# Kernel tuning notes

Measured on AMD Instinct MI355X. Metric: run time of the kernel, lower is better.

Reference implementation:

```python
import jax, jax.numpy as jnp
import numpy as np
from math import sqrt


def setup_inputs() -> dict:
    key = jax.random.key(0)
    kq, kk, kv = jax.random.split(key, 3)
    B, L, H, E = 4, 2048, 8, 64
    S, D = L, E
    return {
        "queries": jax.random.normal(kq, (B, L, H, E), dtype=jnp.float32),
        "keys": jax.random.normal(kk, (B, S, H, E), dtype=jnp.float32),
        "values": jax.random.normal(kv, (B, S, H, D), dtype=jnp.float32),
    }


def reference(queries, keys, values):
    # FullAttention with mask_flag=True (TriangularCausalMask), dropout p=0,
    # output_attention=False. scale = 1/sqrt(E).
    B, L, H, E = queries.shape
    S = keys.shape[1]
    scale = 1.0 / sqrt(E)
    # scores: [B, H, L, S]
    scores = jnp.einsum("blhe,bshe->bhls", queries, keys)
    # causal mask: positions s > l are masked (upper triangle above diagonal)
    causal = jnp.tril(jnp.ones((L, S), dtype=bool))  # True = keep
    neg_inf = jnp.finfo(scores.dtype).min
    scores = jnp.where(causal, scores, neg_inf)
    A = jax.nn.softmax(scale * scores, axis=-1)  # [B,H,L,S]
    # context: [B, L, H, D]
    V = jnp.einsum("bhls,bshd->blhd", A, values)
    return V
```

## Files before the change

kernel.cpp:

```cpp
#include <hip/hip_runtime.h>
#include <math.h>

#define BD 4
#define LD 2048
#define HD 8
#define ED 64
#define TQ 64
#define TK 64
#define RS (HD * ED)
#define NT 32
#define TILE_BYTES 8192

typedef __attribute__((ext_vector_type(8))) _Float16 f16x8;
typedef __attribute__((ext_vector_type(4))) _Float16 f16x4;
typedef __attribute__((ext_vector_type(4))) float f32x4;
typedef __attribute__((ext_vector_type(4))) unsigned int u32x4;
typedef __attribute__((ext_vector_type(2))) unsigned int u32x2;
typedef unsigned int u32;
typedef unsigned long long u64;

__device__ inline u32 pkh(float a, float b) {
    return __builtin_bit_cast(u32, __builtin_amdgcn_cvt_pkrtz(a, b));
}
__device__ inline u64 pkh4(float a, float b, float c, float d) {
    return (u64)pkh(a, b) | ((u64)pkh(c, d) << 32);
}
__device__ inline int swz(int row, int bcol) {
    return row * 128 + ((((bcol >> 4) ^ row) & 7) << 4) + (bcol & 15);
}
__device__ __forceinline__ void gload_lds16(const char* g, char* l) {
    __builtin_amdgcn_global_load_lds(
        (const __attribute__((address_space(1))) unsigned int*)g,
        (__attribute__((address_space(3))) unsigned int*)l, 16, 0, 0);
}

__global__ __launch_bounds__(256, 4)
void cvt_kv(const float* __restrict__ K, const float* __restrict__ V,
            char* __restrict__ Kimg, char* __restrict__ Vimg) {
    const int t  = threadIdx.x;
    const int b  = blockIdx.x >> 3;
    const int h  = blockIdx.x & 7;
    const int kt = blockIdx.y;

    const int ks  = t >> 2;
    const int ke0 = (t & 3) << 2;
    const int vs0 = (t & 15) << 2;
    const int vd0 = (t >> 4) << 2;

    const size_t tb = ((size_t)((b * HD + h) * NT + kt)) * TILE_BYTES;
    char* kd = Kimg + tb;
    char* vd = Vimg + tb;

    const float* kp = K + ((size_t)((b * LD + kt * TK + ks) * HD + h)) * ED + ke0;
    const float* vp = V + ((size_t)((b * LD + kt * TK + vs0) * HD + h)) * ED + vd0;

    float4 kx[4], vx[4];
    #pragma unroll
    for (int j = 0; j < 4; ++j) kx[j] = *(const float4*)(kp + 16 * j);
    #pragma unroll
    for (int r = 0; r < 4; ++r) vx[r] = *(const float4*)(vp + r * RS);

    #pragma unroll
    for (int j = 0; j < 4; ++j)
        *(u64*)(kd + swz(ks, 2 * (ke0 + 16 * j))) = pkh4(kx[j].x, kx[j].y, kx[j].z, kx[j].w);
    *(u64*)(vd + swz(vd0 + 0, 2 * vs0)) = pkh4(vx[0].x, vx[1].x, vx[2].x, vx[3].x);
    *(u64*)(vd + swz(vd0 + 1, 2 * vs0)) = pkh4(vx[0].y, vx[1].y, vx[2].y, vx[3].y);
    *(u64*)(vd + swz(vd0 + 2, 2 * vs0)) = pkh4(vx[0].z, vx[1].z, vx[2].z, vx[3].z);
    *(u64*)(vd + swz(vd0 + 3, 2 * vs0)) = pkh4(vx[0].w, vx[1].w, vx[2].w, vx[3].w);
}

__global__ __launch_bounds__(256, 3)
void fa_f16img(const char* __restrict__ Kimg, const char* __restrict__ Vimg,
               const float* __restrict__ Q, float* __restrict__ O) {
    __shared__ __align__(16) char smem[33792];

    const int t    = threadIdx.x;
    const int lane = t & 63;
    const int w    = t >> 6;
    const int m16  = lane & 15;
    const int quad = lane >> 4;

    const int b = blockIdx.x >> 3;
    const int h = blockIdx.x & 7;
    const int y  = (int)blockIdx.y;
    const int r  = y & 7;
    const int c  = y >> 3;
    const int qt = (c == 0) ? (31 - r) : (c == 1) ? (r + 8)
                 : (c == 2) ? (23 - r) : r;
    const int q0  = qt * TQ;
    const int len = qt + 1;

    const char* Kt = Kimg + (size_t)(b * HD + h) * NT * TILE_BYTES;
    const char* Vt = Vimg + (size_t)(b * HD + h) * NT * TILE_BYTES;
    const int lsrc = (w << 10) + (lane << 4);
    const int ldst = (w << 10);

    #pragma unroll
    for (int inst = 0; inst < 2; ++inst) {
        gload_lds16(Kt + inst * 4096 + lsrc, smem + inst * 4096 + ldst);
        gload_lds16(Vt + inst * 4096 + lsrc, smem + 16384 + inst * 4096 + ldst);
    }

    const float qscale = 0.125f * 1.44269504088896340736f;
    f16x8 qf[4][2];
    #pragma unroll
    for (int qs = 0; qs < 4; ++qs) {
        const float* qrow =
            Q + ((size_t)((b * LD + q0 + (qs << 4) + m16) * HD + h)) * ED;
        #pragma unroll
        for (int hf = 0; hf < 2; ++hf) {
            const float4 x  = *(const float4*)(qrow + hf * 32 + quad * 8);
            const float4 y4 = *(const float4*)(qrow + hf * 32 + quad * 8 + 4);
            u32x4 p;
            p[0] = pkh(x.x * qscale, x.y * qscale);
            p[1] = pkh(x.z * qscale, x.w * qscale);
            p[2] = pkh(y4.x * qscale, y4.y * qscale);
            p[3] = pkh(y4.z * qscale, y4.w * qscale);
            qf[qs][hf] = __builtin_bit_cast(f16x8, p);
        }
    }

    f32x4 oacc[4][4];
    float l_i[4] = {0.f, 0.f, 0.f, 0.f};
    #pragma unroll
    for (int dt = 0; dt < 4; ++dt)
        #pragma unroll
        for (int qs = 0; qs < 4; ++qs) oacc[dt][qs] = (f32x4){0.f, 0.f, 0.f, 0.f};

    const int swK0 = swz((w << 4) + m16, quad * 16);
    const int swK1 = swz((w << 4) + m16, 64 + quad * 16);
    int swV[4];
    #pragma unroll
    for (int dt = 0; dt < 4; ++dt)
        swV[dt] = swz(dt * 16 + m16, (w << 5) + (quad << 3));

    __syncthreads();

    for (int kt = 0; kt < len; ++kt) {
        char* rK = smem + ((kt & 1) << 13);
        char* rV = smem + 16384 + ((kt & 1) << 13);

        if (kt < len - 1) {
            const char* ksrc = Kt + (size_t)(kt + 1) * TILE_BYTES;
            const char* vsrc = Vt + (size_t)(kt + 1) * TILE_BYTES;
            const int bo = ((kt & 1) ^ 1) << 13;
            #pragma unroll
            for (int inst = 0; inst < 2; ++inst) {
                gload_lds16(ksrc + inst * 4096 + lsrc, smem + bo + inst * 4096 + ldst);
                gload_lds16(vsrc + inst * 4096 + lsrc, smem + 16384 + bo + inst * 4096 + ldst);
            }
        }

        const f16x8 kf0 = *(const f16x8*)(rK + swK0);
        const f16x8 kf1 = *(const f16x8*)(rK + swK1);
        f16x4 vf[4];
        #pragma unroll
        for (int dt = 0; dt < 4; ++dt)
            vf[dt] = *(const f16x4*)(rV + swV[dt]);

        const bool diag = (kt == qt);
        #pragma unroll
        for (int qs = 0; qs < 4; ++qs) {
            f32x4 z = {0.f, 0.f, 0.f, 0.f};
            z = __builtin_amdgcn_mfma_f32_16x16x32_f16(kf0, qf[qs][0], z, 0, 0, 0);
            z = __builtin_amdgcn_mfma_f32_16x16x32_f16(kf1, qf[qs][1], z, 0, 0, 0);

            if (diag) {
                const int ql = (qs << 4) + m16;
                const int sl = (w << 4) + (quad << 2);
                #pragma unroll
                for (int i = 0; i < 4; ++i)
                    if (sl + i > ql) z[i] = -INFINITY;
            }

            float p0 = __builtin_amdgcn_exp2f(z[0]);
            float p1 = __builtin_amdgcn_exp2f(z[1]);
            float p2 = __builtin_amdgcn_exp2f(z[2]);
            float p3 = __builtin_amdgcn_exp2f(z[3]);
            l_i[qs] += (p0 + p1) + (p2 + p3);
            u32x2 pp;
            pp[0] = pkh(p0, p1);
            pp[1] = pkh(p2, p3);
            const f16x4 pf = __builtin_bit_cast(f16x4, pp);

            #pragma unroll
            for (int dt = 0; dt < 4; ++dt)
                oacc[dt][qs] = __builtin_amdgcn_mfma_f32_16x16x16f16(vf[dt], pf, oacc[dt][qs], 0, 0, 0);
        }

        __syncthreads();
    }

    #pragma unroll
    for (int qs = 0; qs < 4; ++qs) {
        float l = l_i[qs];
        l += __shfl_xor(l, 16);
        l += __shfl_xor(l, 32);
        l_i[qs] = l;
    }
    float* lbuf = (float*)(smem + 32768);
    if (quad == 0) {
        #pragma unroll
        for (int qs = 0; qs < 4; ++qs)
            lbuf[(w << 6) + (qs << 4) + m16] = l_i[qs];
    }
    if (w >= 2) {
        char* reg = smem + ((w - 2) << 14);
        #pragma unroll
        for (int dt = 0; dt < 4; ++dt)
            #pragma unroll
            for (int qs = 0; qs < 4; ++qs)
                *(f32x4*)(reg + ((((dt << 2) | qs)) << 10) + (lane << 4)) = oacc[dt][qs];
    }
    __syncthreads();
    if (w < 2) {
        char* reg = smem + (w << 14);
        #pragma unroll
        for (int dt = 0; dt < 4; ++dt)
            #pragma unroll
            for (int qs = 0; qs < 4; ++qs)
                oacc[dt][qs] += *(const f32x4*)(reg + ((((dt << 2) | qs)) << 10) + (lane << 4));
    }
    __syncthreads();
    if (w == 1) {
        char* reg = smem;
        #pragma unroll
        for (int dt = 0; dt < 4; ++dt)
            #pragma unroll
            for (int qs = 0; qs < 4; ++qs)
                *(f32x4*)(reg + ((((dt << 2) | qs)) << 10) + (lane << 4)) = oacc[dt][qs];
    }
    __syncthreads();
    if (w == 0) {
        char* reg = smem;
        float inv[4];
        #pragma unroll
        for (int qs = 0; qs < 4; ++qs)
            inv[qs] = 1.0f / (lbuf[(qs << 4) + m16] + lbuf[64 + (qs << 4) + m16] +
                              lbuf[128 + (qs << 4) + m16] + lbuf[192 + (qs << 4) + m16]);
        #pragma unroll
        for (int dt = 0; dt < 4; ++dt)
            #pragma unroll
            for (int qs = 0; qs < 4; ++qs)
                oacc[dt][qs] += *(const f32x4*)(reg + ((((dt << 2) | qs)) << 10) + (lane << 4));
        #pragma unroll
        for (int qs = 0; qs < 4; ++qs) {
            float* orow =
                O + ((size_t)((b * LD + q0 + (qs << 4) + m16) * HD + h)) * ED;
            #pragma unroll
            for (int dt = 0; dt < 4; ++dt) {
                float4 o;
                o.x = oacc[dt][qs][0] * inv[qs];
                o.y = oacc[dt][qs][1] * inv[qs];
                o.z = oacc[dt][qs][2] * inv[qs];
                o.w = oacc[dt][qs][3] * inv[qs];
                *(float4*)(orow + dt * 16 + (quad << 2)) = o;
            }
        }
    }
}

__global__ __launch_bounds__(256, 4)
void fa_mfma_q64(const float* __restrict__ Q, const float* __restrict__ K,
                 const float* __restrict__ V, float* __restrict__ O) {
    __shared__ __align__(16) char smem[32768];
    const int t = threadIdx.x, lane = t & 63, w = t >> 6;
    const int m16 = lane & 15, quad = lane >> 4;
    const int b = blockIdx.x >> 3, h = blockIdx.x & 7;
    const int y = (int)blockIdx.y, r = y & 7, c = y >> 3;
    const int qt = (c == 0) ? (31 - r) : (c == 1) ? (r + 8) : (c == 2) ? (23 - r) : r;
    const int q0 = qt * TQ;
    const int len = qt + 1;
    const int ks = t >> 2, ke0 = (t & 3) << 2;
    const int vs0 = (t & 15) << 2, vd0 = (t >> 4) << 2;
    const float* Kbase = K + ((size_t)((b * LD + ks) * HD + h)) * ED + ke0;
    const float* Vbase = V + ((size_t)((b * LD + vs0) * HD + h)) * ED + vd0;
    const float qscale = 0.125f * 1.44269504088896340736f;
    f16x8 qf[2];
    {
        const float* qrow = Q + ((size_t)((b * LD + q0 + (w << 4) + m16) * HD + h)) * ED;
        #pragma unroll
        for (int hf = 0; hf < 2; ++hf) {
            const float4 x = *(const float4*)(qrow + hf * 32 + quad * 8);
            const float4 y4 = *(const float4*)(qrow + hf * 32 + quad * 8 + 4);
            u32x4 p;
            p[0] = pkh(x.x * qscale, x.y * qscale);
            p[1] = pkh(x.z * qscale, x.w * qscale);
            p[2] = pkh(y4.x * qscale, y4.y * qscale);
            p[3] = pkh(y4.z * qscale, y4.w * qscale);
            qf[hf] = __builtin_bit_cast(f16x8, p);
        }
    }
    f32x4 oacc[4];
    float l_i = 0.0f;
    #pragma unroll
    for (int nt = 0; nt < 4; ++nt) oacc[nt] = (f32x4){0.f, 0.f, 0.f, 0.f};
    float4 kx[4], vx[4];
    {
        #pragma unroll
        for (int j = 0; j < 4; ++j) kx[j] = *(const float4*)(Kbase + 16 * j);
        #pragma unroll
        for (int rr = 0; rr < 4; ++rr) vx[rr] = *(const float4*)(Vbase + rr * RS);
        char* wK = smem;
        char* wV = smem + 16384;
        #pragma unroll
        for (int j = 0; j < 4; ++j)
            *(u64*)(wK + swz(ks, 2 * (ke0 + 16 * j))) = pkh4(kx[j].x, kx[j].y, kx[j].z, kx[j].w);
        *(u64*)(wV + swz(vd0 + 0, 2 * vs0)) = pkh4(vx[0].x, vx[1].x, vx[2].x, vx[3].x);
        *(u64*)(wV + swz(vd0 + 1, 2 * vs0)) = pkh4(vx[0].y, vx[1].y, vx[2].y, vx[3].y);
        *(u64*)(wV + swz(vd0 + 2, 2 * vs0)) = pkh4(vx[0].z, vx[1].z, vx[2].z, vx[3].z);
        *(u64*)(wV + swz(vd0 + 3, 2 * vs0)) = pkh4(vx[0].w, vx[1].w, vx[2].w, vx[3].w);
    }
    __syncthreads();
    for (int kt = 0; kt < len; ++kt) {
        char* rK = smem + ((kt & 1) << 13);
        char* rV = smem + 16384 + ((kt & 1) << 13);
        const bool pre = kt < len - 1;
        if (pre) {
            const float* kp = Kbase + (size_t)(kt + 1) * (TK * RS);
            const float* vp = Vbase + (size_t)(kt + 1) * (TK * RS);
            #pragma unroll
            for (int j = 0; j < 4; ++j) kx[j] = *(const float4*)(kp + 16 * j);
            #pragma unroll
            for (int rr = 0; rr < 4; ++rr) vx[rr] = *(const float4*)(vp + rr * RS);
        }
        f32x4 sacc[4];
        #pragma unroll
        for (int kc = 0; kc < 4; ++kc) {
            const f16x8 kf0 = *(const f16x8*)(rK + swz(kc * 16 + m16, quad * 16));
            const f16x8 kf1 = *(const f16x8*)(rK + swz(kc * 16 + m16, 64 + quad * 16));
            f32x4 z = {0.f, 0.f, 0.f, 0.f};
            z = __builtin_amdgcn_mfma_f32_16x16x32_f16(kf0, qf[0], z, 0, 0, 0);
            z = __builtin_amdgcn_mfma_f32_16x16x32_f16(kf1, qf[1], z, 0, 0, 0);
            sacc[kc] = z;
        }
        if (kt == qt) {
            const int ql = (w << 4) + m16;
            #pragma unroll
            for (int kc = 0; kc < 4; ++kc)
                #pragma unroll
                for (int i = 0; i < 4; ++i)
                    if (kc * 16 + quad * 4 + i > ql) sacc[kc][i] = -INFINITY;
        }
        f16x4 pf[4];
        #pragma unroll
        for (int kc = 0; kc < 4; ++kc) {
            float p0 = __builtin_amdgcn_exp2f(sacc[kc][0]);
            float p1 = __builtin_amdgcn_exp2f(sacc[kc][1]);
            float p2 = __builtin_amdgcn_exp2f(sacc[kc][2]);
            float p3 = __builtin_amdgcn_exp2f(sacc[kc][3]);
            l_i += (p0 + p1) + (p2 + p3);
            u32x2 pp;
            pp[0] = pkh(p0, p1);
            pp[1] = pkh(p2, p3);
            pf[kc] = __builtin_bit_cast(f16x4, pp);
        }
        #pragma unroll
        for (int kc = 0; kc < 4; ++kc) {
            #pragma unroll
            for (int dt = 0; dt < 4; ++dt) {
                const f16x4 vf = *(const f16x4*)
                    (rV + swz(dt * 16 + m16, 2 * (kc * 16 + quad * 4)));
                oacc[dt] = __builtin_amdgcn_mfma_f32_16x16x16f16(vf, pf[kc], oacc[dt], 0, 0, 0);
            }
        }
        if (pre) {
            char* wK = smem + ((kt & 1) ? 0 : 8192);
            char* wV = smem + 16384 + ((kt & 1) ? 0 : 8192);
            #pragma unroll
            for (int j = 0; j < 4; ++j)
                *(u64*)(wK + swz(ks, 2 * (ke0 + 16 * j))) = pkh4(kx[j].x, kx[j].y, kx[j].z, kx[j].w);
            *(u64*)(wV + swz(vd0 + 0, 2 * vs0)) = pkh4(vx[0].x, vx[1].x, vx[2].x, vx[3].x);
            *(u64*)(wV + swz(vd0 + 1, 2 * vs0)) = pkh4(vx[0].y, vx[1].y, vx[2].y, vx[3].y);
            *(u64*)(wV + swz(vd0 + 2, 2 * vs0)) = pkh4(vx[0].z, vx[1].z, vx[2].z, vx[3].z);
            *(u64*)(wV + swz(vd0 + 3, 2 * vs0)) = pkh4(vx[0].w, vx[1].w, vx[2].w, vx[3].w);
        }
        __syncthreads();
    }
    {
        float l = l_i;
        l += __shfl_xor(l, 16);
        l += __shfl_xor(l, 32);
        const float inv = 1.0f / l;
        float* orow = O + ((size_t)((b * LD + q0 + (w << 4) + m16) * HD + h)) * ED;
        #pragma unroll
        for (int dt = 0; dt < 4; ++dt) {
            float4 o;
            o.x = oacc[dt][0] * inv;
            o.y = oacc[dt][1] * inv;
            o.z = oacc[dt][2] * inv;
            o.w = oacc[dt][3] * inv;
            *(float4*)(orow + dt * 16 + quad * 4) = o;
        }
    }
}

extern "C" void kernel_launch(void* const* d_in, const int* in_sizes, int n_in,
                              void* d_out, int out_size, void* d_ws, size_t ws_size,
                              hipStream_t stream) {
    const float* Q = (const float*)d_in[0];
    const float* K = (const float*)d_in[1];
    const float* V = (const float*)d_in[2];
    float* O = (float*)d_out;

    const size_t img = (size_t)BD * HD * NT * TILE_BYTES;
    if (d_ws != nullptr && ws_size >= 2 * img) {
        char* Kimg = (char*)d_ws;
        char* Vimg = (char*)d_ws + img;
        cvt_kv<<<dim3(BD * HD, NT), 256, 0, stream>>>(K, V, Kimg, Vimg);
        fa_f16img<<<dim3(BD * HD, 32), 256, 0, stream>>>(Kimg, Vimg, Q, O);
    } else {
        fa_mfma_q64<<<dim3(BD * HD, 32), 256, 0, stream>>>(Q, K, V, O);
    }
}
```

Baseline: 120.7 us.

## Triple-buffer K/V tiles with vmcnt-based waits and one barrier per iteration

Replaces the double-buffered K/V LDS pipeline with a three-stage ring. Loads now run two tiles ahead, and each iteration starts with a manual s_waitcnt vmcnt(4) plus one barrier instead of a trailing __syncthreads. The goal is to hide global-to-LDS latency better and drop one synchronisation point per iteration. Shared memory grows from about 33KB to 49KB per block, which may lower occupancy below the 3 blocks per CU that the launch bounds target. Redundant clamped loads are issued at the tail.

```diff
diff --git a/kernel.cpp b/kernel.cpp
--- a/kernel.cpp
+++ b/kernel.cpp
@@ -72,7 +72,7 @@
 __global__ __launch_bounds__(256, 3)
 void fa_f16img(const char* __restrict__ Kimg, const char* __restrict__ Vimg,
                const float* __restrict__ Q, float* __restrict__ O) {
-    __shared__ __align__(16) char smem[33792];
+    __shared__ __align__(16) char smem[50176];
 
     const int t    = threadIdx.x;
     const int lane = t & 63;
@@ -95,10 +95,23 @@
     const int lsrc = (w << 10) + (lane << 4);
     const int ldst = (w << 10);
 
-    #pragma unroll
-    for (int inst = 0; inst < 2; ++inst) {
-        gload_lds16(Kt + inst * 4096 + lsrc, smem + inst * 4096 + ldst);
-        gload_lds16(Vt + inst * 4096 + lsrc, smem + 16384 + inst * 4096 + ldst);
+
+    {
+        const char* k0 = Kt;
+        const char* v0 = Vt;
+        #pragma unroll
+        for (int inst = 0; inst < 2; ++inst) {
+            gload_lds16(k0 + inst * 4096 + lsrc, smem + inst * 4096 + ldst);
+            gload_lds16(v0 + inst * 4096 + lsrc, smem + 24576 + inst * 4096 + ldst);
+        }
+        const int t1 = (1 <= len - 1) ? 1 : 0;
+        const char* k1 = Kt + (size_t)t1 * TILE_BYTES;
+        const char* v1 = Vt + (size_t)t1 * TILE_BYTES;
+        #pragma unroll
+        for (int inst = 0; inst < 2; ++inst) {
+            gload_lds16(k1 + inst * 4096 + lsrc, smem + 8192 + inst * 4096 + ldst);
+            gload_lds16(v1 + inst * 4096 + lsrc, smem + 24576 + 8192 + inst * 4096 + ldst);
+        }
     }
 
     const float qscale = 0.125f * 1.44269504088896340736f;
@@ -134,22 +147,28 @@
     for (int dt = 0; dt < 4; ++dt)
         swV[dt] = swz(dt * 16 + m16, (w << 5) + (quad << 3));
 
-    __syncthreads();
-
+    int buf = 0;
     for (int kt = 0; kt < len; ++kt) {
-        char* rK = smem + ((kt & 1) << 13);
-        char* rV = smem + 16384 + ((kt & 1) << 13);
-
-        if (kt < len - 1) {
-            const char* ksrc = Kt + (size_t)(kt + 1) * TILE_BYTES;
-            const char* vsrc = Vt + (size_t)(kt + 1) * TILE_BYTES;
-            const int bo = ((kt & 1) ^ 1) << 13;
+        asm volatile("s_waitcnt vmcnt(4)" ::: "memory");
+        __builtin_amdgcn_s_barrier();
+        __builtin_amdgcn_sched_barrier(0);
+
+        {
+            const int tn = (kt + 2 <= len - 1) ? (kt + 2) : (len - 1);
+            const int bn = (buf + 2 >= 3) ? (buf - 1) : (buf + 2);
+            const char* ksrc = Kt + (size_t)tn * TILE_BYTES;
+            const char* vsrc = Vt + (size_t)tn * TILE_BYTES;
+            char* kd = smem + bn * 8192;
+            char* vd = smem + 24576 + bn * 8192;
             #pragma unroll
             for (int inst = 0; inst < 2; ++inst) {
-                gload_lds16(ksrc + inst * 4096 + lsrc, smem + bo + inst * 4096 + ldst);
-                gload_lds16(vsrc + inst * 4096 + lsrc, smem + 16384 + bo + inst * 4096 + ldst);
+                gload_lds16(ksrc + inst * 4096 + lsrc, kd + inst * 4096 + ldst);
+                gload_lds16(vsrc + inst * 4096 + lsrc, vd + inst * 4096 + ldst);
             }
         }
+
+        char* rK = smem + buf * 8192;
+        char* rV = smem + 24576 + buf * 8192;
 
         const f16x8 kf0 = *(const f16x8*)(rK + swK0);
         const f16x8 kf1 = *(const f16x8*)(rK + swK1);
@@ -188,8 +207,10 @@
                 oacc[dt][qs] = __builtin_amdgcn_mfma_f32_16x16x16f16(vf[dt], pf, oacc[dt][qs], 0, 0, 0);
         }
 
-        __syncthreads();
-    }
+        buf = (buf == 2) ? 0 : (buf + 1);
+    }
+
+    __syncthreads();
 
     #pragma unroll
     for (int qs = 0; qs < 4; ++qs) {
@@ -198,7 +219,7 @@
         l += __shfl_xor(l, 32);
         l_i[qs] = l;
     }
-    float* lbuf = (float*)(smem + 32768);
+    float* lbuf = (float*)(smem + 49152);
     if (quad == 0) {
         #pragma unroll
         for (int qs = 0; qs < 4; ++qs)
```

Measured after the change: 124.0 us. 2.8% more time.

## Load K/V fragments directly from global into registers with prefetch, dropping LDS staging

Applied to the files above, without the earlier changes.

The attention loop no longer stages K/V tiles through double-buffered LDS via global_load_lds with a block barrier each iteration. Each wave now reads its swizzled fragments straight from the pre-converted global image into registers and prefetches the next tile one iteration ahead. The aim is to remove per-tile __syncthreads and LDS round trips. The cost is more live registers (the launch bound drops from 3 to 2 blocks per CU) and reliance on cache for data shared across waves.

```diff
diff --git a/kernel.cpp b/kernel.cpp
--- a/kernel.cpp
+++ b/kernel.cpp
@@ -28,11 +28,6 @@
 __device__ inline int swz(int row, int bcol) {
     return row * 128 + ((((bcol >> 4) ^ row) & 7) << 4) + (bcol & 15);
 }
-__device__ __forceinline__ void gload_lds16(const char* g, char* l) {
-    __builtin_amdgcn_global_load_lds(
-        (const __attribute__((address_space(1))) unsigned int*)g,
-        (__attribute__((address_space(3))) unsigned int*)l, 16, 0, 0);
-}
 
 __global__ __launch_bounds__(256, 4)
 void cvt_kv(const float* __restrict__ K, const float* __restrict__ V,
@@ -69,7 +64,7 @@
     *(u64*)(vd + swz(vd0 + 3, 2 * vs0)) = pkh4(vx[0].w, vx[1].w, vx[2].w, vx[3].w);
 }
 
-__global__ __launch_bounds__(256, 3)
+__global__ __launch_bounds__(256, 2)
 void fa_f16img(const char* __restrict__ Kimg, const char* __restrict__ Vimg,
                const float* __restrict__ Q, float* __restrict__ O) {
     __shared__ __align__(16) char smem[33792];
@@ -92,14 +87,13 @@
 
     const char* Kt = Kimg + (size_t)(b * HD + h) * NT * TILE_BYTES;
     const char* Vt = Vimg + (size_t)(b * HD + h) * NT * TILE_BYTES;
-    const int lsrc = (w << 10) + (lane << 4);
-    const int ldst = (w << 10);
-
-    #pragma unroll
-    for (int inst = 0; inst < 2; ++inst) {
-        gload_lds16(Kt + inst * 4096 + lsrc, smem + inst * 4096 + ldst);
-        gload_lds16(Vt + inst * 4096 + lsrc, smem + 16384 + inst * 4096 + ldst);
-    }
+
+    const int swK0 = swz((w << 4) + m16, quad * 16);
+    const int swK1 = swz((w << 4) + m16, 64 + quad * 16);
+    int swV[4];
+    #pragma unroll
+    for (int dt = 0; dt < 4; ++dt)
+        swV[dt] = swz(dt * 16 + m16, (w << 5) + (quad << 3));
 
     const float qscale = 0.125f * 1.44269504088896340736f;
     f16x8 qf[4][2];
@@ -127,43 +121,31 @@
         #pragma unroll
         for (int qs = 0; qs < 4; ++qs) oacc[dt][qs] = (f32x4){0.f, 0.f, 0.f, 0.f};
 
-    const int swK0 = swz((w << 4) + m16, quad * 16);
-    const int swK1 = swz((w << 4) + m16, 64 + quad * 16);
-    int swV[4];
+    f16x8 kc0 = *(const f16x8*)(Kt + swK0);
+    f16x8 kc1 = *(const f16x8*)(Kt + swK1);
+    f16x4 vc[4];
     #pragma unroll
     for (int dt = 0; dt < 4; ++dt)
-        swV[dt] = swz(dt * 16 + m16, (w << 5) + (quad << 3));
-
-    __syncthreads();
+        vc[dt] = *(const f16x4*)(Vt + swV[dt]);
 
     for (int kt = 0; kt < len; ++kt) {
-        char* rK = smem + ((kt & 1) << 13);
-        char* rV = smem + 16384 + ((kt & 1) << 13);
-
-        if (kt < len - 1) {
-            const char* ksrc = Kt + (size_t)(kt + 1) * TILE_BYTES;
-            const char* vsrc = Vt + (size_t)(kt + 1) * TILE_BYTES;
-            const int bo = ((kt & 1) ^ 1) << 13;
-            #pragma unroll
-            for (int inst = 0; inst < 2; ++inst) {
-                gload_lds16(ksrc + inst * 4096 + lsrc, smem + bo + inst * 4096 + ldst);
-                gload_lds16(vsrc + inst * 4096 + lsrc, smem + 16384 + bo + inst * 4096 + ldst);
-            }
-        }
-
-        const f16x8 kf0 = *(const f16x8*)(rK + swK0);
-        const f16x8 kf1 = *(const f16x8*)(rK + swK1);
-        f16x4 vf[4];
+        const int ktn = (kt + 1 < len) ? (kt + 1) : kt;
+        const char* kb = Kt + (size_t)ktn * TILE_BYTES;
+        const char* vb = Vt + (size_t)ktn * TILE_BYTES;
+        f16x8 kn0 = *(const f16x8*)(kb + swK0);
+        f16x8 kn1 = *(const f16x8*)(kb + swK1);
+        f16x4 vn[4];
         #pragma unroll
         for (int dt = 0; dt < 4; ++dt)
-            vf[dt] = *(const f16x4*)(rV + swV[dt]);
+            vn[dt] = *(const f16x4*)(vb + swV[dt]);
+        __builtin_amdgcn_sched_barrier(0);
 
         const bool diag = (kt == qt);
         #pragma unroll
         for (int qs = 0; qs < 4; ++qs) {
             f32x4 z = {0.f, 0.f, 0.f, 0.f};
-            z = __builtin_amdgcn_mfma_f32_16x16x32_f16(kf0, qf[qs][0], z, 0, 0, 0);
-            z = __builtin_amdgcn_mfma_f32_16x16x32_f16(kf1, qf[qs][1], z, 0, 0, 0);
+            z = __builtin_amdgcn_mfma_f32_16x16x32_f16(kc0, qf[qs][0], z, 0, 0, 0);
+            z = __builtin_amdgcn_mfma_f32_16x16x32_f16(kc1, qf[qs][1], z, 0, 0, 0);
 
             if (diag) {
                 const int ql = (qs << 4) + m16;
@@ -185,10 +167,13 @@
 
             #pragma unroll
             for (int dt = 0; dt < 4; ++dt)
-                oacc[dt][qs] = __builtin_amdgcn_mfma_f32_16x16x16f16(vf[dt], pf, oacc[dt][qs], 0, 0, 0);
-        }
-
-        __syncthreads();
+                oacc[dt][qs] = __builtin_amdgcn_mfma_f32_16x16x16f16(vc[dt], pf, oacc[dt][qs], 0, 0, 0);
+        }
+
+        kc0 = kn0;
+        kc1 = kn1;
+        #pragma unroll
+        for (int dt = 0; dt < 4; ++dt) vc[dt] = vn[dt];
     }
 
     #pragma unroll
```

New measurement: 123.0 us. About the same (+2.0%).
